# Kernel optimization log

Hardware: AMD Instinct MI355X
Metric: run time of the kernel (lower is better)

Reference implementation:

```python
import jax, jax.numpy as jnp
import numpy as np

N_NODES = 50000
N_EDGES = 800000
D_IN = 128
D_HID = 128


def setup_inputs() -> dict:
    key = jax.random.key(0)
    ks = jax.random.split(key, 9)
    x = jax.random.normal(ks[0], (N_NODES, D_IN), dtype=jnp.float32)
    edge_index = jax.random.randint(ks[1], (2, N_EDGES), 0, N_NODES, dtype=jnp.int64)
    s = 1.0 / np.sqrt(D_IN)
    # SAGEConv params: lin_l acts on mean-aggregated neighbors (has bias),
    # lin_r acts on the root/self features (no bias). Stored as [in, out].
    Wl1 = jax.random.uniform(ks[2], (D_IN, D_HID), jnp.float32, -s, s)
    Wr1 = jax.random.uniform(ks[3], (D_IN, D_HID), jnp.float32, -s, s)
    b1 = jax.random.uniform(ks[4], (D_HID,), jnp.float32, -s, s)
    Wl2 = jax.random.uniform(ks[5], (D_HID, D_HID), jnp.float32, -s, s)
    Wr2 = jax.random.uniform(ks[6], (D_HID, D_HID), jnp.float32, -s, s)
    b2 = jax.random.uniform(ks[7], (D_HID,), jnp.float32, -s, s)
    return {"x": x, "edge_index": edge_index, "Wl1": Wl1, "Wr1": Wr1,
            "b1": b1, "Wl2": Wl2, "Wr2": Wr2, "b2": b2}


def _sage_conv(h, src, dst, n_nodes, Wl, Wr, b):
    # gather neighbor features, mean-aggregate at targets (PyG mean aggr)
    msg = h[src]  # [E, d]
    summed = jax.ops.segment_sum(msg, dst, num_segments=n_nodes)  # [N, d]
    cnt = jax.ops.segment_sum(jnp.ones((src.shape[0], 1), h.dtype), dst,
                              num_segments=n_nodes)  # [N, 1]
    agg = summed / jnp.maximum(cnt, 1.0)  # isolated nodes -> 0, matches scatter-mean
    return agg @ Wl + b + h @ Wr


def reference(x, edge_index, Wl1, Wr1, b1, Wl2, Wr2, b2):
    src = edge_index[0]  # source nodes j (messages flow j -> i)
    dst = edge_index[1]  # target nodes i
    n = x.shape[0]
    h = _sage_conv(x, src, dst, n, Wl1, Wr1, b1)
    h = jax.nn.relu(h)  # dropout is identity in eval mode
    out = _sage_conv(h, src, dst, n, Wl2, Wr2, b2)
    return out
```

## Files before the change

kernel.cpp:

```cpp
#include <hip/hip_runtime.h>
#include <hip/hip_bf16.h>

#define DD 128
#define BSH 8
#define CHUNK 4096

typedef __attribute__((ext_vector_type(8))) short short8v;
typedef __attribute__((ext_vector_type(4))) float f32x4;

static __device__ __forceinline__ ushort f2bf(float f) {
    __hip_bfloat16 b = __float2bfloat16(f);
    return *reinterpret_cast<ushort*>(&b);
}


__global__ __launch_bounds__(256) void k_prep(const int* __restrict__ ei,
                                              int* __restrict__ hist, int E, int NB, int nblk,
                                              const float* __restrict__ x,
                                              ushort* __restrict__ xbf, int n4, int castBlocks,
                                              const float* __restrict__ Wl1,
                                              const float* __restrict__ Wr1,
                                              ushort* __restrict__ Wt1,
                                              const float* __restrict__ Wl2,
                                              const float* __restrict__ Wr2,
                                              ushort* __restrict__ Wt2) {
    __shared__ int lh[256];
    int t = threadIdx.x;
    int b = blockIdx.x;

    if (b < nblk) {
        lh[t] = 0;
        __syncthreads();
        int e0 = b * CHUNK;
        int e1 = min(e0 + CHUNK, E);
        for (int e = e0 + t; e < e1; e += 256)
            atomicAdd(&lh[ei[E + e] >> BSH], 1);
        __syncthreads();
        if (t < NB) hist[b * NB + t] = lh[t];
        return;
    }
    b -= nblk;
    if (b < castBlocks) {
        int i = b * 256 + t;
        if (i < n4) {
            float4 v = reinterpret_cast<const float4*>(x)[i];
            ushort4 o;
            o.x = f2bf(v.x); o.y = f2bf(v.y); o.z = f2bf(v.z); o.w = f2bf(v.w);
            reinterpret_cast<ushort4*>(xbf)[i] = o;
        }
        return;
    }
    b -= castBlocks;
    {
        const float* Wl = (b < 128) ? Wl1 : Wl2;
        const float* Wr = (b < 128) ? Wr1 : Wr2;
        ushort* Wt = (b < 128) ? Wt1 : Wt2;
        int idx = (b & 127) * 256 + t;
        int nn = idx >> 8, k = idx & 255;
        float v = (k < 128) ? Wl[k * 128 + nn] : Wr[(k - 128) * 128 + nn];
        Wt[nn * 256 + k] = f2bf(v);
    }
}

__global__ __launch_bounds__(1024) void k_hscan(int* __restrict__ hist,
                                                int* __restrict__ bbase,
                                                int nblk, int NB, int E) {
    __shared__ int part[4][256];
    __shared__ int s[256];
    int t = threadIdx.x;
    int b = t & 255, g = t >> 8;
    int q = (nblk + 3) >> 2;
    int lo = g * q, hi = min(lo + q, nblk);
    int sum = 0;
    if (b < NB)
        for (int blk = lo; blk < hi; ++blk) sum += hist[blk * NB + b];
    part[g][b] = sum;
    __syncthreads();
    if (g == 0) s[b] = part[0][b] + part[1][b] + part[2][b] + part[3][b];
    __syncthreads();
    for (int off = 1; off < 256; off <<= 1) {
        int v = 0;
        if (g == 0 && b >= off) v = s[b - off];
        __syncthreads();
        if (g == 0) s[b] += v;
        __syncthreads();
    }
    int base = (b == 0) ? 0 : s[b - 1];
    if (g == 0 && b < NB) bbase[b] = base;
    if (t == 0) bbase[NB] = E;
    int run = base;
    for (int gg = 0; gg < g; ++gg) run += part[gg][b];
    if (b < NB)
        for (int blk = lo; blk < hi; ++blk) {
            int tmp = hist[blk * NB + b];
            hist[blk * NB + b] = run;
            run += tmp;
        }
}

__global__ __launch_bounds__(256) void k_scatter(const int* __restrict__ ei,
                                                 const int* __restrict__ hist,
                                                 uint* __restrict__ pairs, int E, int NB) {
    __shared__ int lofs[256];
    __shared__ int lh[256];
    int t = threadIdx.x;
    int blk = blockIdx.x;
    lh[t] = 0;
    if (t < NB) lofs[t] = hist[blk * NB + t];
    __syncthreads();
    int e0 = blk * CHUNK, e1 = min(e0 + CHUNK, E);
    for (int e = e0 + t; e < e1; e += 256) {
        int sN = ei[e];
        int d = ei[E + e];
        int b = d >> BSH;
        int lp = atomicAdd(&lh[b], 1);
        pairs[lofs[b] + lp] = ((uint)(d & 255) << 16) | (uint)sN;
    }
}

__global__ __launch_bounds__(256) void k_csr(const uint* __restrict__ pairs,
                                             const int* __restrict__ bbase,
                                             int* __restrict__ rowptr,
                                             ushort* __restrict__ eidx,
                                             int n, int E, int NB) {
    __shared__ int lc[256];
    __shared__ int cur[256];
    int t = threadIdx.x;
    int b = blockIdx.x;
    int node0 = b << BSH;
    lc[t] = 0;
    __syncthreads();
    int r0 = bbase[b], r1 = bbase[b + 1];
    for (int i = r0 + t; i < r1; i += 256)
        atomicAdd(&lc[pairs[i] >> 16], 1);
    __syncthreads();
    int c0 = lc[t];
#pragma unroll
    for (int off = 1; off < 256; off <<= 1) {
        int u = (t >= off) ? lc[t - off] : 0;
        __syncthreads();
        lc[t] += u;
        __syncthreads();
    }
    int rp = r0 + lc[t] - c0;
    int node = node0 + t;
    if (node < n) rowptr[node] = rp;
    if (b == NB - 1 && t == 0) rowptr[n] = E;
    cur[t] = rp;
    __syncthreads();
    for (int i = r0 + t; i < r1; i += 256) {
        uint pr = pairs[i];
        int p = atomicAdd(&cur[pr >> 16], 1);
        eidx[p] = (ushort)(pr & 0xFFFFu);
    }
}


#define ACC8(v)                                    \
    acc[0] += __uint_as_float((v).x << 16);        \
    acc[1] += __uint_as_float((v).x & 0xffff0000u);\
    acc[2] += __uint_as_float((v).y << 16);        \
    acc[3] += __uint_as_float((v).y & 0xffff0000u);\
    acc[4] += __uint_as_float((v).z << 16);        \
    acc[5] += __uint_as_float((v).z & 0xffff0000u);\
    acc[6] += __uint_as_float((v).w << 16);        \
    acc[7] += __uint_as_float((v).w & 0xffff0000u);

__global__ __launch_bounds__(512, 6) void k_fused(const ushort* __restrict__ hin,
                                                  const int* __restrict__ rowptr,
                                                  const ushort* __restrict__ eidx,
                                                  const ushort* __restrict__ Wt,
                                                  const float* __restrict__ bias,
                                                  void* __restrict__ outp,
                                                  int n, int relu, int outBf16) {
    __shared__ ushort sagg[32][128];
    __shared__ ushort sroot[32][128];

    int t = threadIdx.x;
    int node0 = blockIdx.x * 32;

    {
        int r = t >> 4, c = t & 15;
        int row = node0 + r;
        if (row >= n) row = n - 1;
        uint4 v = *reinterpret_cast<const uint4*>(hin + (size_t)row * DD + c * 8);
        int cs = c ^ (r & 15);
        *reinterpret_cast<uint4*>(&sroot[r][cs * 8]) = v;
    }

    int wave = t >> 6;
    int lane = t & 63;
    int grp = lane >> 4;
    int c16 = lane & 15;
    {
        int node = node0 + wave * 4 + grp;
        int beg = 0, end = 0;
        if (node < n) { beg = rowptr[node]; end = rowptr[node + 1]; }
        const uint4* base = reinterpret_cast<const uint4*>(hin);

        float acc[8];
#pragma unroll
        for (int i = 0; i < 8; ++i) acc[i] = 0.f;

        int e = beg;
        for (; e + 8 <= end; e += 8) {
            int id[8];
            uint4 v[8];
#pragma unroll
            for (int j = 0; j < 8; ++j) id[j] = eidx[e + j];
#pragma unroll
            for (int j = 0; j < 8; ++j) v[j] = base[(size_t)id[j] * 16 + c16];
#pragma unroll
            for (int j = 0; j < 8; ++j) { ACC8(v[j]); }
        }
        for (; e < end; e += 4) {
            int m = end - e;
            int i0 = eidx[e];
            int i1 = eidx[e + (m > 1 ? 1 : 0)];
            int i2 = eidx[e + (m > 2 ? 2 : 0)];
            int i3 = eidx[e + (m > 3 ? 3 : 0)];
            uint4 v0 = base[(size_t)i0 * 16 + c16];
            uint4 v1 = base[(size_t)i1 * 16 + c16];
            uint4 v2 = base[(size_t)i2 * 16 + c16];
            uint4 v3 = base[(size_t)i3 * 16 + c16];
            ACC8(v0);
            if (m > 1) { ACC8(v1); }
            if (m > 2) { ACC8(v2); }
            if (m > 3) { ACC8(v3); }
        }

        float inv = 1.0f / fmaxf((float)(end - beg), 1.0f);
        uint4 o;
        o.x = ((uint)f2bf(acc[1] * inv) << 16) | (uint)f2bf(acc[0] * inv);
        o.y = ((uint)f2bf(acc[3] * inv) << 16) | (uint)f2bf(acc[2] * inv);
        o.z = ((uint)f2bf(acc[5] * inv) << 16) | (uint)f2bf(acc[4] * inv);
        o.w = ((uint)f2bf(acc[7] * inv) << 16) | (uint)f2bf(acc[6] * inv);
        int r = wave * 4 + grp;
        int cs = c16 ^ (r & 15);
        *reinterpret_cast<uint4*>(&sagg[r][cs * 8]) = o;
    }
    __syncthreads();

    int lr = lane & 15;
    int lk = lane >> 4;
    int nt = wave;

    short8v bf[8];
    const ushort* wbase = Wt + (size_t)(nt * 16 + lr) * 256 + lk * 8;
#pragma unroll
    for (int ks = 0; ks < 8; ++ks)
        bf[ks] = *reinterpret_cast<const short8v*>(wbase + ks * 32);

    int col = nt * 16 + lr;
    float bv = bias[col];

#pragma unroll
    for (int sub = 0; sub < 2; ++sub) {
        int m0 = sub * 16;
        int r = m0 + lr;
        f32x4 acc = (f32x4){0.f, 0.f, 0.f, 0.f};
#pragma unroll
        for (int ks = 0; ks < 4; ++ks) {
            int cc = ks * 4 + lk;
            int cs = cc ^ (r & 15);
            short8v af = *reinterpret_cast<const short8v*>(&sagg[r][cs * 8]);
            acc = __builtin_amdgcn_mfma_f32_16x16x32_bf16(af, bf[ks], acc, 0, 0, 0);
        }
#pragma unroll
        for (int ks = 0; ks < 4; ++ks) {
            int cc = ks * 4 + lk;
            int cs = cc ^ (r & 15);
            short8v af = *reinterpret_cast<const short8v*>(&sroot[r][cs * 8]);
            acc = __builtin_amdgcn_mfma_f32_16x16x32_bf16(af, bf[ks + 4], acc, 0, 0, 0);
        }

        int rowb = node0 + m0 + lk * 4;
#pragma unroll
        for (int q = 0; q < 4; ++q) {
            int row = rowb + q;
            if (row < n) {
                float v = acc[q] + bv;
                if (relu) v = fmaxf(v, 0.f);
                if (outBf16) {
                    reinterpret_cast<ushort*>(outp)[(size_t)row * DD + col] = f2bf(v);
                } else {
                    reinterpret_cast<float*>(outp)[(size_t)row * DD + col] = v;
                }
            }
        }
    }
}


extern "C" void kernel_launch(void* const* d_in, const int* in_sizes, int n_in,
                              void* d_out, int out_size, void* d_ws, size_t ws_size,
                              hipStream_t stream) {
    const float* x   = (const float*)d_in[0];
    const int*   ei  = (const int*)d_in[1];
    const float* Wl1 = (const float*)d_in[2];
    const float* Wr1 = (const float*)d_in[3];
    const float* b1  = (const float*)d_in[4];
    const float* Wl2 = (const float*)d_in[5];
    const float* Wr2 = (const float*)d_in[6];
    const float* b2  = (const float*)d_in[7];
    float* out = (float*)d_out;

    int n = in_sizes[0] / DD;
    int E = in_sizes[1] / 2;

    int NB   = (n + 255) >> 8;
    int nblk = (E + CHUNK - 1) / CHUNK;

    char* ws = (char*)d_ws;
    size_t off = 0;
    auto take = [&](size_t bytes) -> void* {
        void* p = ws + off;
        off = (off + bytes + 255) & ~(size_t)255;
        return p;
    };
    int* rowptr    = (int*)take(((size_t)n + 1) * 4);
    int* hist      = (int*)take((size_t)nblk * NB * 4);
    int* bbase     = (int*)take(((size_t)NB + 1) * 4);
    ushort* eidx   = (ushort*)take((size_t)E * 2 + 16);
    uint* pairs    = (uint*)take((size_t)E * 4);
    ushort* xbf    = (ushort*)take((size_t)n * DD * 2);
    ushort* hbf    = (ushort*)take((size_t)n * DD * 2);
    ushort* Wt1    = (ushort*)take((size_t)DD * 256 * 2);
    ushort* Wt2    = (ushort*)take((size_t)DD * 256 * 2);

    int n4 = n * DD / 4;
    int castBlocks = (n4 + 255) / 256;
    int prepBlocks = nblk + castBlocks + 256;

    k_prep<<<prepBlocks, 256, 0, stream>>>(ei, hist, E, NB, nblk,
                                           x, xbf, n4, castBlocks,
                                           Wl1, Wr1, Wt1, Wl2, Wr2, Wt2);
    k_hscan<<<1, 1024, 0, stream>>>(hist, bbase, nblk, NB, E);
    k_scatter<<<nblk, 256, 0, stream>>>(ei, hist, pairs, E, NB);
    k_csr<<<NB, 256, 0, stream>>>(pairs, bbase, rowptr, eidx, n, E, NB);

    int fusedBlocks = (n + 31) / 32;

    k_fused<<<fusedBlocks, 512, 0, stream>>>(xbf, rowptr, eidx, Wt1, b1, hbf, n, 1, 1);
    k_fused<<<fusedBlocks, 512, 0, stream>>>(hbf, rowptr, eidx, Wt2, b2, out, n, 0, 0);
}
```

Measured before the change: 154.1 us.

## Split neighbor gather across edge slots with shuffle reduction per column quarter

The aggregation loop now assigns 4 lanes per edge slot, so each 16-lane group fetches four neighbors in parallel. Each pass covers one 32-column quarter of the feature row, four passes in total, and partial sums are combined with xor shuffles. This is meant to raise memory-level parallelism for low-degree nodes and cut register pressure, and launch bounds are raised to allow 8 waves. The cost is four passes over the edge list (re-reading eidx), a __syncthreads per pass, and shuffle reduction overhead.

```diff
diff --git a/kernel.cpp b/kernel.cpp
--- a/kernel.cpp
+++ b/kernel.cpp
@@ -166,7 +166,7 @@
     acc[6] += __uint_as_float((v).w << 16);        \
     acc[7] += __uint_as_float((v).w & 0xffff0000u);
 
-__global__ __launch_bounds__(512, 6) void k_fused(const ushort* __restrict__ hin,
+__global__ __launch_bounds__(512, 8) void k_fused(const ushort* __restrict__ hin,
                                                   const int* __restrict__ rowptr,
                                                   const ushort* __restrict__ eidx,
                                                   const ushort* __restrict__ Wt,
@@ -191,55 +191,61 @@
     int wave = t >> 6;
     int lane = t & 63;
     int grp = lane >> 4;
-    int c16 = lane & 15;
-    {
-        int node = node0 + wave * 4 + grp;
-        int beg = 0, end = 0;
-        if (node < n) { beg = rowptr[node]; end = rowptr[node + 1]; }
-        const uint4* base = reinterpret_cast<const uint4*>(hin);
-
+    int sub16 = lane & 15;
+    int eslot = sub16 >> 2;
+    int ch = sub16 & 3;
+    int r = wave * 4 + grp;
+
+    int node = node0 + r;
+    int beg = 0, end = 0;
+    if (node < n) { beg = rowptr[node]; end = rowptr[node + 1]; }
+    float inv = 1.0f / fmaxf((float)(end - beg), 1.0f);
+
+#pragma unroll
+    for (int q = 0; q < 4; ++q) {
         float acc[8];
 #pragma unroll
         for (int i = 0; i < 8; ++i) acc[i] = 0.f;
 
+        int qo = q * 32 + ch * 8;
         int e = beg;
-        for (; e + 8 <= end; e += 8) {
-            int id[8];
-            uint4 v[8];
-#pragma unroll
-            for (int j = 0; j < 8; ++j) id[j] = eidx[e + j];
-#pragma unroll
-            for (int j = 0; j < 8; ++j) v[j] = base[(size_t)id[j] * 16 + c16];
-#pragma unroll
-            for (int j = 0; j < 8; ++j) { ACC8(v[j]); }
+        for (; e + 16 <= end; e += 16) {
+            uint4 v[4];
+#pragma unroll
+            for (int s = 0; s < 4; ++s) {
+                int id = eidx[e + s * 4 + eslot];
+                v[s] = *reinterpret_cast<const uint4*>(hin + (size_t)id * DD + qo);
+            }
+#pragma unroll
+            for (int s = 0; s < 4; ++s) { ACC8(v[s]); }
         }
         for (; e < end; e += 4) {
-            int m = end - e;
-            int i0 = eidx[e];
-            int i1 = eidx[e + (m > 1 ? 1 : 0)];
-            int i2 = eidx[e + (m > 2 ? 2 : 0)];
-            int i3 = eidx[e + (m > 3 ? 3 : 0)];
-            uint4 v0 = base[(size_t)i0 * 16 + c16];
-            uint4 v1 = base[(size_t)i1 * 16 + c16];
-            uint4 v2 = base[(size_t)i2 * 16 + c16];
-            uint4 v3 = base[(size_t)i3 * 16 + c16];
-            ACC8(v0);
-            if (m > 1) { ACC8(v1); }
-            if (m > 2) { ACC8(v2); }
-            if (m > 3) { ACC8(v3); }
-        }
-
-        float inv = 1.0f / fmaxf((float)(end - beg), 1.0f);
-        uint4 o;
-        o.x = ((uint)f2bf(acc[1] * inv) << 16) | (uint)f2bf(acc[0] * inv);
-        o.y = ((uint)f2bf(acc[3] * inv) << 16) | (uint)f2bf(acc[2] * inv);
-        o.z = ((uint)f2bf(acc[5] * inv) << 16) | (uint)f2bf(acc[4] * inv);
-        o.w = ((uint)f2bf(acc[7] * inv) << 16) | (uint)f2bf(acc[6] * inv);
-        int r = wave * 4 + grp;
-        int cs = c16 ^ (r & 15);
-        *reinterpret_cast<uint4*>(&sagg[r][cs * 8]) = o;
-    }
-    __syncthreads();
+            int ee = e + eslot;
+            if (ee < end) {
+                int id = eidx[ee];
+                uint4 v0 = *reinterpret_cast<const uint4*>(hin + (size_t)id * DD + qo);
+                ACC8(v0);
+            }
+        }
+
+#pragma unroll
+        for (int i = 0; i < 8; ++i) {
+            acc[i] += __shfl_xor(acc[i], 4);
+            acc[i] += __shfl_xor(acc[i], 8);
+        }
+
+        if (eslot == 0) {
+            uint4 o;
+            o.x = ((uint)f2bf(acc[1] * inv) << 16) | (uint)f2bf(acc[0] * inv);
+            o.y = ((uint)f2bf(acc[3] * inv) << 16) | (uint)f2bf(acc[2] * inv);
+            o.z = ((uint)f2bf(acc[5] * inv) << 16) | (uint)f2bf(acc[4] * inv);
+            o.w = ((uint)f2bf(acc[7] * inv) << 16) | (uint)f2bf(acc[6] * inv);
+            int cc = q * 4 + ch;
+            int cs = cc ^ (r & 15);
+            *reinterpret_cast<uint4*>(&sagg[r][cs * 8]) = o;
+        }
+        __syncthreads();
+    }
 
     int lr = lane & 15;
     int lk = lane >> 4;
@@ -257,29 +263,29 @@
 #pragma unroll
     for (int sub = 0; sub < 2; ++sub) {
         int m0 = sub * 16;
-        int r = m0 + lr;
+        int rr = m0 + lr;
         f32x4 acc = (f32x4){0.f, 0.f, 0.f, 0.f};
 #pragma unroll
         for (int ks = 0; ks < 4; ++ks) {
             int cc = ks * 4 + lk;
-            int cs = cc ^ (r & 15);
-            short8v af = *reinterpret_cast<const short8v*>(&sagg[r][cs * 8]);
+            int cs = cc ^ (rr & 15);
+            short8v af = *reinterpret_cast<const short8v*>(&sagg[rr][cs * 8]);
             acc = __builtin_amdgcn_mfma_f32_16x16x32_bf16(af, bf[ks], acc, 0, 0, 0);
         }
 #pragma unroll
         for (int ks = 0; ks < 4; ++ks) {
             int cc = ks * 4 + lk;
-            int cs = cc ^ (r & 15);
-            short8v af = *reinterpret_cast<const short8v*>(&sroot[r][cs * 8]);
+            int cs = cc ^ (rr & 15);
+            short8v af = *reinterpret_cast<const short8v*>(&sroot[rr][cs * 8]);
             acc = __builtin_amdgcn_mfma_f32_16x16x32_bf16(af, bf[ks + 4], acc, 0, 0, 0);
         }
 
         int rowb = node0 + m0 + lk * 4;
 #pragma unroll
-        for (int q = 0; q < 4; ++q) {
-            int row = rowb + q;
+        for (int qq = 0; qq < 4; ++qq) {
+            int row = rowb + qq;
             if (row < n) {
-                float v = acc[q] + bv;
+                float v = acc[qq] + bv;
                 if (relu) v = fmaxf(v, 0.f);
                 if (outBf16) {
                     reinterpret_cast<ushort*>(outp)[(size_t)row * DD + col] = f2bf(v);
```

New measurement: 177.6 us. 15.3% more time.

## Sort nodes by degree before fused SAGE kernels to balance per-block work

Applied to the files above, without the earlier changes.

Adds three small kernels that bin nodes by in-degree (capped at 63) and build a permutation grouping nodes of similar degree together. The fused aggregation+MFMA kernels then process nodes in permuted order, reading rowptr and writing output through the permutation. The goal is to cut load imbalance across the 16-lane groups within a wave and across blocks. The cost is three extra launches, a memset, and scattered row writes and root loads in place of contiguous ones. Padded slots in the last block write duplicate copies of row n-1, which is harmless.

```diff
diff --git a/kernel.cpp b/kernel.cpp
--- a/kernel.cpp
+++ b/kernel.cpp
@@ -156,6 +156,60 @@
 }
 
 
+__global__ __launch_bounds__(256) void k_dhist(const int* __restrict__ rowptr,
+                                               int* __restrict__ dbin, int n) {
+    __shared__ int lh[64];
+    int t = threadIdx.x;
+    if (t < 64) lh[t] = 0;
+    __syncthreads();
+    int i = blockIdx.x * 256 + t;
+    if (i < n) {
+        int d = rowptr[i + 1] - rowptr[i];
+        if (d > 63) d = 63;
+        atomicAdd(&lh[d], 1);
+    }
+    __syncthreads();
+    if (t < 64) atomicAdd(&dbin[t], lh[t]);
+}
+
+__global__ void k_dscan(const int* __restrict__ dbin, int* __restrict__ dcur) {
+    __shared__ int s[64];
+    int t = threadIdx.x;
+    s[t] = dbin[t];
+    __syncthreads();
+    for (int off = 1; off < 64; off <<= 1) {
+        int v = (t >= off) ? s[t - off] : 0;
+        __syncthreads();
+        s[t] += v;
+        __syncthreads();
+    }
+    dcur[t] = (t == 0) ? 0 : s[t - 1];
+}
+
+__global__ __launch_bounds__(256) void k_dfill(const int* __restrict__ rowptr,
+                                               int* __restrict__ dcur,
+                                               int* __restrict__ perm, int n) {
+    __shared__ int lh[64], lbase[64];
+    int t = threadIdx.x;
+    if (t < 64) lh[t] = 0;
+    __syncthreads();
+    int i = blockIdx.x * 256 + t;
+    int d = -1;
+    if (i < n) {
+        d = rowptr[i + 1] - rowptr[i];
+        if (d > 63) d = 63;
+        atomicAdd(&lh[d], 1);
+    }
+    __syncthreads();
+    if (t < 64) { lbase[t] = atomicAdd(&dcur[t], lh[t]); lh[t] = 0; }
+    __syncthreads();
+    if (i < n) {
+        int lp = atomicAdd(&lh[d], 1);
+        perm[lbase[d] + lp] = i;
+    }
+}
+
+
 #define ACC8(v)                                    \
     acc[0] += __uint_as_float((v).x << 16);        \
     acc[1] += __uint_as_float((v).x & 0xffff0000u);\
@@ -169,20 +223,27 @@
 __global__ __launch_bounds__(512, 6) void k_fused(const ushort* __restrict__ hin,
                                                   const int* __restrict__ rowptr,
                                                   const ushort* __restrict__ eidx,
+                                                  const int* __restrict__ perm,
                                                   const ushort* __restrict__ Wt,
                                                   const float* __restrict__ bias,
                                                   void* __restrict__ outp,
                                                   int n, int relu, int outBf16) {
     __shared__ ushort sagg[32][128];
     __shared__ ushort sroot[32][128];
+    __shared__ int sperm[32];
 
     int t = threadIdx.x;
     int node0 = blockIdx.x * 32;
+
+    if (t < 32) {
+        int slot = node0 + t;
+        sperm[t] = (slot < n) ? perm[slot] : (n - 1);
+    }
+    __syncthreads();
 
     {
         int r = t >> 4, c = t & 15;
-        int row = node0 + r;
-        if (row >= n) row = n - 1;
+        int row = sperm[r];
         uint4 v = *reinterpret_cast<const uint4*>(hin + (size_t)row * DD + c * 8);
         int cs = c ^ (r & 15);
         *reinterpret_cast<uint4*>(&sroot[r][cs * 8]) = v;
@@ -193,9 +254,8 @@
     int grp = lane >> 4;
     int c16 = lane & 15;
     {
-        int node = node0 + wave * 4 + grp;
-        int beg = 0, end = 0;
-        if (node < n) { beg = rowptr[node]; end = rowptr[node + 1]; }
+        int node = sperm[wave * 4 + grp];
+        int beg = rowptr[node], end = rowptr[node + 1];
         const uint4* base = reinterpret_cast<const uint4*>(hin);
 
         float acc[8];
@@ -274,18 +334,16 @@
             acc = __builtin_amdgcn_mfma_f32_16x16x32_bf16(af, bf[ks + 4], acc, 0, 0, 0);
         }
 
-        int rowb = node0 + m0 + lk * 4;
+        int slotb = m0 + lk * 4;
 #pragma unroll
         for (int q = 0; q < 4; ++q) {
-            int row = rowb + q;
-            if (row < n) {
-                float v = acc[q] + bv;
-                if (relu) v = fmaxf(v, 0.f);
-                if (outBf16) {
-                    reinterpret_cast<ushort*>(outp)[(size_t)row * DD + col] = f2bf(v);
-                } else {
-                    reinterpret_cast<float*>(outp)[(size_t)row * DD + col] = v;
-                }
+            int row = sperm[slotb + q];
+            float v = acc[q] + bv;
+            if (relu) v = fmaxf(v, 0.f);
+            if (outBf16) {
+                reinterpret_cast<ushort*>(outp)[(size_t)row * DD + col] = f2bf(v);
+            } else {
+                reinterpret_cast<float*>(outp)[(size_t)row * DD + col] = v;
             }
         }
     }
@@ -321,6 +379,9 @@
     int* rowptr    = (int*)take(((size_t)n + 1) * 4);
     int* hist      = (int*)take((size_t)nblk * NB * 4);
     int* bbase     = (int*)take(((size_t)NB + 1) * 4);
+    int* dbin      = (int*)take(64 * 4);
+    int* dcur      = (int*)take(64 * 4);
+    int* perm      = (int*)take((size_t)n * 4);
     ushort* eidx   = (ushort*)take((size_t)E * 2 + 16);
     uint* pairs    = (uint*)take((size_t)E * 4);
     ushort* xbf    = (ushort*)take((size_t)n * DD * 2);
@@ -331,16 +392,22 @@
     int n4 = n * DD / 4;
     int castBlocks = (n4 + 255) / 256;
     int prepBlocks = nblk + castBlocks + 256;
+    int nodeBlocks = (n + 255) / 256;
 
     k_prep<<<prepBlocks, 256, 0, stream>>>(ei, hist, E, NB, nblk,
                                            x, xbf, n4, castBlocks,
                                            Wl1, Wr1, Wt1, Wl2, Wr2, Wt2);
+    hipMemsetAsync(dbin, 0, 64 * 4, stream);
     k_hscan<<<1, 1024, 0, stream>>>(hist, bbase, nblk, NB, E);
     k_scatter<<<nblk, 256, 0, stream>>>(ei, hist, pairs, E, NB);
     k_csr<<<NB, 256, 0, stream>>>(pairs, bbase, rowptr, eidx, n, E, NB);
 
+    k_dhist<<<nodeBlocks, 256, 0, stream>>>(rowptr, dbin, n);
+    k_dscan<<<1, 64, 0, stream>>>(dbin, dcur);
+    k_dfill<<<nodeBlocks, 256, 0, stream>>>(rowptr, dcur, perm, n);
+
     int fusedBlocks = (n + 31) / 32;
 
-    k_fused<<<fusedBlocks, 512, 0, stream>>>(xbf, rowptr, eidx, Wt1, b1, hbf, n, 1, 1);
-    k_fused<<<fusedBlocks, 512, 0, stream>>>(hbf, rowptr, eidx, Wt2, b2, out, n, 0, 0);
-}
+    k_fused<<<fusedBlocks, 512, 0, stream>>>(xbf, rowptr, eidx, perm, Wt1, b1, hbf, n, 1, 1);
+    k_fused<<<fusedBlocks, 512, 0, stream>>>(hbf, rowptr, eidx, perm, Wt2, b2, out, n, 0, 0);
+}
```

Result: no change. 154.3 us (+0.1%).
